# Kernel optimization log

Hardware: AMD Instinct MI355X
Metric: run time of the kernel (lower is better)

Reference implementation:

```python
import jax, jax.numpy as jnp
import numpy as np

EPS = 1e-9
TOP_K = 2
CAPACITY_FACTOR = 4.0
MIN_EXPERT_CAPACITY = 4


def setup_inputs() -> dict:
    key = jax.random.key(0)
    k1, k2 = jax.random.split(key)
    x = jax.random.normal(k1, (4, 32, 512, 24, 24), dtype=jnp.float32)
    w_gating = jax.random.normal(k2, (512, 16), dtype=jnp.float32)
    return {"x": x, "w_gating": w_gating}


def cumsum_exclusive(t, axis):
    # exclusive cumsum along `axis`: cumsum shifted by one (zero first)
    return jnp.cumsum(t, axis=axis) - t


def reference(x, w_gating):
    T, B, D, H, W = x.shape
    N = H * W                       # group_size (tokens per image)
    E = w_gating.shape[1]           # num_gates / experts
    dt = x.dtype

    # pool over timesteps: (T,B,D,H,W) -> (B,N,D)
    x_tok = x.reshape(T, B, D, N).transpose(0, 1, 3, 2)
    x_pooled = x_tok.mean(axis=0)

    raw_gates = jax.nn.softmax(jnp.einsum('bnd,de->bne', x_pooled, w_gating), axis=-1)

    # --- top-k selection loop (importance=None, so no importance masking) ---
    gates_remaining = raw_gates
    masks, gates, indices = [], [], []
    for k in range(TOP_K):
        index_k = jnp.argmax(gates_remaining, axis=-1)                 # (B,N)
        gate_k = jnp.take_along_axis(gates_remaining, index_k[..., None], axis=-1)[..., 0]
        mask_k = jax.nn.one_hot(index_k, E, dtype=dt)                  # (B,N,E)
        masks.append(mask_k)
        gates.append(gate_k)
        indices.append(index_k)
        gates_remaining = gates_remaining * (1.0 - mask_k)

    gate_sum = sum(gates) + EPS
    gates = [g / gate_sum for g in gates]

    # load-balancing loss
    density_1 = masks[0].mean(axis=-2)          # (B,E)
    density_1_proxy = raw_gates.mean(axis=-2)   # (B,E)
    loss = (density_1_proxy * density_1).mean() * float(E ** 2)

    # policy == 'all': masks unchanged

    expert_capacity = min(N, int(N * CAPACITY_FACTOR / E))
    expert_capacity = max(expert_capacity, MIN_EXPERT_CAPACITY)
    cap_f = float(expert_capacity)

    # --- capacity assignment ---
    cumulative_position = jnp.zeros((B, 1, E), dtype=dt)
    positions = [None] * TOP_K
    for k in range(TOP_K):
        position_k = cumsum_exclusive(masks[k], axis=-2) + cumulative_position
        position_k = position_k * masks[k]
        masks[k] = masks[k] * (position_k < cap_f).astype(dt)
        positions[k] = position_k.sum(axis=-1)                          # (B,N)
        gates[k] = gates[k] * masks[k].sum(axis=-1)
        cumulative_position = cumulative_position + masks[k].sum(axis=-2, keepdims=True)

    # --- combine / dispatch tensors (B, N, E, C) ---
    combine_tensor = jnp.zeros((B, N, E, expert_capacity), dtype=dt)
    for k in range(TOP_K):
        mask_k_flat = masks[k].sum(axis=-1)                             # (B,N)
        expert_oh = jax.nn.one_hot(indices[k], E, dtype=dt)             # (B,N,E)
        # out-of-range positions produce all-zero rows, matching safe_one_hot's slice
        pos_oh = jax.nn.one_hot(positions[k].astype(jnp.int32), expert_capacity, dtype=dt)  # (B,N,C)
        combine_tensor = combine_tensor + (
            (gates[k] * mask_k_flat)[..., None, None]
            * expert_oh[..., None]
            * pos_oh[..., None, :]
        )
    dispatch_tensor = (combine_tensor != 0).astype(dt)
    return dispatch_tensor, combine_tensor, loss
```

## Files before the change

kernel.cpp:

```cpp
#include <hip/hip_runtime.h>

#define TT 4
#define BB 32
#define DD 512
#define NN 576
#define EE 16
#define DC 8
#define DCH 64
#define CC 144
#define ROW (EE*CC)
#define SZ 42467328UL
#define Z4PB 82944
#define Z4PT 144

typedef float f4 __attribute__((ext_vector_type(4)));

__global__ __launch_bounds__(576) void k_partzero(const float* __restrict__ x,
                                                  const float* __restrict__ w,
                                                  float* __restrict__ part,
                                                  float* __restrict__ out) {
  const int b  = blockIdx.x;
  const int dc = blockIdx.y;
  const int n  = threadIdx.x;
  const int d0 = dc * DCH;

  f4* outz = (f4*)out;
  const size_t zbase = (size_t)(b + dc * BB) * Z4PB + n;
  const f4 zv = {0.f, 0.f, 0.f, 0.f};

  float acc[EE];
#pragma unroll
  for (int e = 0; e < EE; ++e) acc[e] = 0.f;

  for (int t = 0; t < TT; ++t) {
    const float* xp = x + (((size_t)t * BB + b) * DD + d0) * NN + n;
    for (int dd = 0; dd < DCH; dd += 8) {
      float xv[8];
#pragma unroll
      for (int u = 0; u < 8; ++u) xv[u] = xp[(size_t)(dd + u) * NN];
#pragma unroll
      for (int u = 0; u < 8; ++u) {
        const float* wd = w + (size_t)(d0 + dd + u) * EE;
#pragma unroll
        for (int e = 0; e < EE; ++e) acc[e] = fmaf(xv[u], wd[e], acc[e]);
      }
    }
#pragma unroll 4
    for (int k = t * 36; k < t * 36 + 36; ++k)
      outz[zbase + (size_t)k * 576] = zv;
  }

  float4* dst4 = (float4*)(part + (((size_t)b * NN + n) * DC + dc) * EE);
#pragma unroll
  for (int q = 0; q < 4; ++q)
    dst4[q] = make_float4(acc[4*q], acc[4*q+1], acc[4*q+2], acc[4*q+3]);
}

__global__ __launch_bounds__(576) void k_gate(const float* __restrict__ part,
                                              float4* __restrict__ info,
                                              float* __restrict__ lossp) {
  const int b = blockIdx.x;
  const int n = threadIdx.x;
  const int wave = n >> 6, lane = n & 63;

  __shared__ float sprox[9][EE];
  __shared__ int   swc1[9][EE];
  __shared__ int   swc2[9][EE];
  __shared__ int   woff1[9][EE];
  __shared__ int   woff2[9][EE];
  __shared__ float sproxTot[EE];
  __shared__ int   scnt0[EE];
  __shared__ int   sbase2[EE];

  float l[EE];
#pragma unroll
  for (int e = 0; e < EE; ++e) l[e] = 0.f;
  {
    const float4* p4 = (const float4*)(part + (size_t)(b * NN + n) * (DC * EE));
#pragma unroll
    for (int dc = 0; dc < DC; ++dc) {
#pragma unroll
      for (int q = 0; q < 4; ++q) {
        float4 v = p4[dc * 4 + q];
        l[4*q+0] += v.x; l[4*q+1] += v.y; l[4*q+2] += v.z; l[4*q+3] += v.w;
      }
    }
#pragma unroll
    for (int e = 0; e < EE; ++e) l[e] *= 0.25f;
  }

  float m = l[0];
#pragma unroll
  for (int e = 1; e < EE; ++e) m = fmaxf(m, l[e]);
  float raw[EE]; float s = 0.f;
#pragma unroll
  for (int e = 0; e < EE; ++e) { raw[e] = expf(l[e] - m); s += raw[e]; }
  float inv = 1.f / s;
#pragma unroll
  for (int e = 0; e < EE; ++e) raw[e] *= inv;

  int e1 = 0; float g1 = raw[0];
#pragma unroll
  for (int e = 1; e < EE; ++e) if (raw[e] > g1) { g1 = raw[e]; e1 = e; }
  int e2 = (e1 == 0) ? 1 : 0; float g2 = raw[e2];
#pragma unroll
  for (int e = 0; e < EE; ++e) if (e != e1 && raw[e] > g2) { g2 = raw[e]; e2 = e; }
  const float denom = g1 + g2 + 1e-9f;
  const float w0 = g1 / denom, w1 = g2 / denom;

  const unsigned long long ltm = (1ull << lane) - 1ull;
  int pre1 = 0, pre2 = 0;
#pragma unroll
  for (int e = 0; e < EE; ++e) {
    unsigned long long m1 = __ballot(e1 == e);
    unsigned long long m2 = __ballot(e2 == e);
    if (lane == 0) { swc1[wave][e] = __popcll(m1); swc2[wave][e] = __popcll(m2); }
    if (e == e1) pre1 = __popcll(m1 & ltm);
    if (e == e2) pre2 = __popcll(m2 & ltm);
  }

#pragma unroll
  for (int e = 0; e < EE; ++e) {
    float v = raw[e];
#pragma unroll
    for (int off = 32; off; off >>= 1) v += __shfl_xor(v, off);
    if (lane == 0) sprox[wave][e] = v;
  }
  __syncthreads();

  if (n < EE) {
    int r1 = 0, r2 = 0; float pv = 0.f;
#pragma unroll
    for (int wv = 0; wv < 9; ++wv) {
      woff1[wv][n] = r1; r1 += swc1[wv][n];
      woff2[wv][n] = r2; r2 += swc2[wv][n];
      pv += sprox[wv][n];
    }
    scnt0[n]    = r1;
    sbase2[n]   = r1 < CC ? r1 : CC;
    sproxTot[n] = pv;
  }
  __syncthreads();

  if (n == 0) {
    float S = 0.f;
    for (int e = 0; e < EE; ++e) S += sproxTot[e] * (float)scnt0[e];
    lossp[b] = S / ((float)NN * (float)NN);
  }

  const int p0 = woff1[wave][e1] + pre1;
  const int p1 = sbase2[e2] + woff2[wave][e2] + pre2;

  const int  pos0 = (p0 < CC) ? (e1 * CC + p0) : -1;
  const int  pos1 = (p1 < CC) ? (e2 * CC + p1) : -1;
  const float w0k = (p0 < CC) ? w0 : 0.f;
  const float w1k = (p1 < CC) ? w1 : 0.f;

  float4 o;
  o.x = __int_as_float(pos0);
  o.y = w0k;
  o.z = __int_as_float(pos1);
  o.w = w1k;
  info[b * NN + n] = o;
}

__global__ __launch_bounds__(512) void k_scatter(const float4* __restrict__ info,
                                                 const float* __restrict__ lossp,
                                                 float* __restrict__ out) {
  const int tok = blockIdx.x * 512 + threadIdx.x;
  if (tok == 0) {
    float sv = 0.f;
    for (int b = 0; b < BB; ++b) sv += lossp[b];
    out[2 * SZ] = 0.5f * sv;
  }
  const float4 inf = info[tok];
  const int   pos0 = __float_as_int(inf.x);
  const int   pos1 = __float_as_int(inf.z);

  float* disp = out + (size_t)tok * ROW;
  float* comb = out + SZ + (size_t)tok * ROW;
  if (pos0 >= 0) { disp[pos0] = 1.f; comb[pos0] = inf.y; }
  if (pos1 >= 0) { disp[pos1] = 1.f; comb[pos1] = inf.w; }
}

extern "C" void kernel_launch(void* const* d_in, const int* in_sizes, int n_in,
                              void* d_out, int out_size, void* d_ws, size_t ws_size,
                              hipStream_t stream) {
  const float* x = (const float*)d_in[0];
  const float* w = (const float*)d_in[1];
  float* out = (float*)d_out;

  float*  part  = (float*)d_ws;
  float4* info  = (float4*)((char*)d_ws + 9437184);
  float*  lossp = (float*)((char*)d_ws + 9437184 + 294912);

  hipLaunchKernelGGL(k_partzero, dim3(BB, DC), dim3(576), 0, stream, x, w, part, out);
  hipLaunchKernelGGL(k_gate,     dim3(BB),     dim3(576), 0, stream, part, info, lossp);
  hipLaunchKernelGGL(k_scatter,  dim3(36),     dim3(512), 0, stream, info, lossp, out);
}
```

Measured before the change: 138.0 us.

## Split zero-fill into dedicated blocks and pre-sum timesteps before gating FMAs

The fused kernel now launches 512 blocks. Blocks 0-255 compute the gating partial sums and blocks 256-511 only zero-fill the output, where before every block interleaved both jobs. The reduction loop loads all four timesteps for a given d together, adds them, and then does one set of 16 FMAs, which cuts FMA count by four. The aim is to let memory-bound zero stores and x reads run on separate CUs concurrently and to reduce ALU work. In exchange the summation order changes slightly and the two block types may be unevenly loaded.

Result: no change. 137.3 us (-0.5%).

```diff
diff --git a/kernel.cpp b/kernel.cpp
--- a/kernel.cpp
+++ b/kernel.cpp
@@ -10,8 +10,7 @@
 #define CC 144
 #define ROW (EE*CC)
 #define SZ 42467328UL
-#define Z4PB 82944
-#define Z4PT 144
+#define ZF4PB 82944
 
 typedef float f4 __attribute__((ext_vector_type(4)));
 
@@ -19,35 +18,41 @@
                                                   const float* __restrict__ w,
                                                   float* __restrict__ part,
                                                   float* __restrict__ out) {
-  const int b  = blockIdx.x;
-  const int dc = blockIdx.y;
-  const int n  = threadIdx.x;
+  const int blk = blockIdx.x;
+  const int n   = threadIdx.x;
+
+  if (blk >= 256) {
+    const int zid = blk - 256;
+    f4* outz = (f4*)out + (size_t)zid * ZF4PB + n;
+    const f4 zv = {0.f, 0.f, 0.f, 0.f};
+#pragma unroll 8
+    for (int k = 0; k < 144; ++k)
+      outz[(size_t)k * 576] = zv;
+    return;
+  }
+
+  const int b  = blk & 31;
+  const int dc = blk >> 5;
   const int d0 = dc * DCH;
 
-  f4* outz = (f4*)out;
-  const size_t zbase = (size_t)(b + dc * BB) * Z4PB + n;
-  const f4 zv = {0.f, 0.f, 0.f, 0.f};
+  const float* xp = x + ((size_t)b * DD + d0) * NN + n;
+  const size_t TS = (size_t)BB * DD * NN;
 
   float acc[EE];
 #pragma unroll
   for (int e = 0; e < EE; ++e) acc[e] = 0.f;
 
-  for (int t = 0; t < TT; ++t) {
-    const float* xp = x + (((size_t)t * BB + b) * DD + d0) * NN + n;
-    for (int dd = 0; dd < DCH; dd += 8) {
-      float xv[8];
-#pragma unroll
-      for (int u = 0; u < 8; ++u) xv[u] = xp[(size_t)(dd + u) * NN];
-#pragma unroll
-      for (int u = 0; u < 8; ++u) {
-        const float* wd = w + (size_t)(d0 + dd + u) * EE;
-#pragma unroll
-        for (int e = 0; e < EE; ++e) acc[e] = fmaf(xv[u], wd[e], acc[e]);
-      }
-    }
-#pragma unroll 4
-    for (int k = t * 36; k < t * 36 + 36; ++k)
-      outz[zbase + (size_t)k * 576] = zv;
+#pragma unroll 2
+  for (int dd = 0; dd < DCH; ++dd) {
+    const size_t o = (size_t)dd * NN;
+    const float x0 = xp[o];
+    const float x1 = xp[o + TS];
+    const float x2 = xp[o + 2 * TS];
+    const float x3 = xp[o + 3 * TS];
+    const float xs = (x0 + x1) + (x2 + x3);
+    const float* wd = w + (size_t)(d0 + dd) * EE;
+#pragma unroll
+    for (int e = 0; e < EE; ++e) acc[e] = fmaf(xs, wd[e], acc[e]);
   }
 
   float4* dst4 = (float4*)(part + (((size_t)b * NN + n) * DC + dc) * EE);
@@ -194,7 +199,7 @@
   float4* info  = (float4*)((char*)d_ws + 9437184);
   float*  lossp = (float*)((char*)d_ws + 9437184 + 294912);
 
-  hipLaunchKernelGGL(k_partzero, dim3(BB, DC), dim3(576), 0, stream, x, w, part, out);
-  hipLaunchKernelGGL(k_gate,     dim3(BB),     dim3(576), 0, stream, part, info, lossp);
-  hipLaunchKernelGGL(k_scatter,  dim3(36),     dim3(512), 0, stream, info, lossp, out);
-}
+  hipLaunchKernelGGL(k_partzero, dim3(512), dim3(576), 0, stream, x, w, part, out);
+  hipLaunchKernelGGL(k_gate,     dim3(BB),  dim3(576), 0, stream, part, info, lossp);
+  hipLaunchKernelGGL(k_scatter,  dim3(36),  dim3(512), 0, stream, info, lossp, out);
+}
```
